# Performance work log

Measured on AMD Instinct MI355X. Metric: run time of the kernel, lower is better.

The kernel has to match this reference:

```python
import jax, jax.numpy as jnp
import numpy as np

P = 16          # patch size
D = 256         # embed dim (complex channels)
L = 2           # depth (num blocks)
NE = 4          # num experts
FF = 1024       # ffn hidden = expand * D
B, T, C, IH, IW = 1, 8, 4, 256, 256
HP, WP = IH // P, IW // P


def setup_inputs():
    key = jax.random.key(0)
    ks = iter(jax.random.split(key, 40))
    r = lambda shape, s=0.02: jax.random.normal(next(ks), shape, jnp.float32) * s
    sD = 1.0 / np.sqrt(D)
    return {
        'x': jax.random.normal(next(ks), (B, T, C, IH, IW), jnp.float32),
        'dt': jax.random.uniform(next(ks), (B, T), jnp.float32, 0.1, 1.0),
        'Wenc': r((C * P * P, 2 * D)),
        'benc': jnp.zeros((2 * D,), jnp.float32),
        'Wdec': r((2 * D, C * P * P)),
        'bdec': jnp.zeros((C * P * P,), jnp.float32),
        'ln_sp_w': jnp.ones((L, 2 * D), jnp.float32),
        'ln_sp_b': jnp.zeros((L, 2 * D), jnp.float32),
        'conv_w': r((L, 2 * D, 2 * D, 3, 3)),
        'conv_b': jnp.zeros((L, 2 * D), jnp.float32),
        'E_re': r((L, D, D), sD), 'E_im': r((L, D, D), sD),
        'Ed_re': r((L, D, D), sD), 'Ed_im': r((L, D, D), sD),
        'Ws_re': r((L, D, D), sD), 'Ws_im': r((L, D, D), sD),
        'Wg': r((L, 2 * D, D)),
        'bg': jnp.zeros((L, D), jnp.float32),
        'lam_re': r((L, D), 1.0), 'lam_im': r((L, D), 1.0),
        'ln_t_w': jnp.ones((L, 2 * D), jnp.float32),
        'ln_t_b': jnp.zeros((L, 2 * D), jnp.float32),
        'Wr': r((L, 2 * D, NE)),
        'W1': r((L, NE, 2 * D, FF)),
        'W2': r((L, NE, FF, 2 * D)),
    }


def _ln(x, w, b):
    m = x.mean(-1, keepdims=True)
    v = ((x - m) ** 2).mean(-1, keepdims=True)
    return (x - m) * jax.lax.rsqrt(v + 1e-5) * w + b


def _block(z, h_prev, flux_prev, dt, bp):
    (ln_sp_w, ln_sp_b, conv_w, conv_b, E_re, E_im, Ed_re, Ed_im,
     Ws_re, Ws_im, Wg, bg, lam_re, lam_im, ln_t_w, ln_t_b, Wr, W1, W2) = bp
    Bq, Tq, Dq, H, W = z.shape
    # --- spatial process: LN + conv on concat(real, imag), complex residual ---
    zf = z.reshape(Bq * Tq, Dq, H, W)
    zr = jnp.concatenate([zf.real, zf.imag], axis=1)
    zn = _ln(zr.transpose(0, 2, 3, 1), ln_sp_w, ln_sp_b).transpose(0, 3, 1, 2)
    zs = jax.lax.conv_general_dilated(zn, conv_w, (1, 1), 'SAME',
                                      dimension_numbers=('NCHW', 'OIHW', 'NCHW'))
    zs = zs + conv_b[None, :, None, None]
    re, im = jnp.split(zs, 2, axis=1)
    x = (zf + (re + 1j * im)).reshape(Bq, Tq, Dq, H, W)
    # --- eigen-basis encode ---
    Eb = E_re + 1j * E_im
    x_eigen = jnp.einsum('btdhw,de->bthwe', x, Eb)   # [B,T,H,W,D] complex
    x_mean = x_eigen.mean(axis=(2, 3))               # [B,T,D] complex
    # --- sequential gated flux recurrence over T ---
    Ws = Ws_re + 1j * Ws_im
    def step(flux, xm):
        source = xm @ Ws
        feat = jnp.concatenate([xm.real, xm.imag], -1)
        gate = jax.nn.sigmoid(feat @ Wg + bg)        # real [B,D]
        new_flux = gate * flux + (1.0 - gate) * source
        return new_flux, (new_flux, source, gate)
    _, (flux_seq, source_seq, gate_seq) = jax.lax.scan(step, flux_prev, x_mean.transpose(1, 0, 2))
    flux_seq = flux_seq.transpose(1, 0, 2)
    source_seq = source_seq.transpose(1, 0, 2)
    gate_seq = gate_seq.transpose(1, 0, 2)
    g = gate_seq[:, :, None, None, :]
    forcing = x_eigen * g + source_seq[:, :, None, None, :] * (1.0 - g)
    # --- transition operators ---
    lam = -(jax.nn.softplus(lam_re) + 1e-2) + 1j * lam_im        # [D]
    op_decay = jnp.exp(lam[None, None, :] * dt[:, :, None])      # [B,T,D] complex
    op_forcing = (op_decay - 1.0) / lam
    a = jnp.broadcast_to(op_decay[:, :, None, None, :], forcing.shape)
    u = forcing * op_forcing[:, :, None, None, :]
    # --- parallel linear scan h_t = a_t * h_{t-1} + u_t along T ---
    def comb(c1, c2):
        a1, u1 = c1
        a2, u2 = c2
        return a1 * a2, u1 * a2 + u2
    _, h = jax.lax.associative_scan(comb, (a, u), axis=1)
    # as written in source: h_prev contribution is h_prev * op_decay at every t
    h = h + h_prev.reshape(Bq, 1, H, W, Dq) * a
    last_h = h[:, -1].reshape(Bq * H * W, 1, Dq)
    last_flux = flux_seq[:, -1]
    # --- eigen decode + temporal LN + MoE FFN ---
    Ed = Ed_re + 1j * Ed_im
    x_out = jnp.einsum('bthwe,ed->btdhw', h, Ed)
    xf = x_out.reshape(Bq * Tq, Dq, H, W)
    xr = jnp.concatenate([xf.real, xf.imag], axis=1)
    xn = _ln(xr.transpose(0, 2, 3, 1), ln_t_w, ln_t_b)           # [BT,H,W,2D]
    tok = xn.reshape(-1, 2 * Dq)
    probs = jax.nn.softmax(tok @ Wr, axis=-1)                    # [N,E]
    hid = jax.nn.gelu(jnp.einsum('nd,edf->nef', tok, W1))
    y = jnp.einsum('nef,efd,ne->nd', hid, W2, probs)             # [N,2D]
    xc = xn[..., :Dq] + 1j * xn[..., Dq:]
    delta = (y[..., :Dq] + 1j * y[..., Dq:]).reshape(Bq * Tq, H, W, Dq)
    x_cplx = (xc + delta).reshape(Bq, Tq, H, W, Dq).transpose(0, 1, 4, 2, 3)
    return x + x_cplx, last_h, last_flux


def _forward(x, dt, Wenc, benc, Wdec, bdec, ln_sp_w, ln_sp_b, conv_w, conv_b,
             E_re, E_im, Ed_re, Ed_im, Ws_re, Ws_im, Wg, bg, lam_re, lam_im,
             ln_t_w, ln_t_b, Wr, W1, W2):
    # encoder: patchify + linear -> complex latent [B,T,D,HP,WP]
    xp = x.reshape(B, T, C, HP, P, WP, P).transpose(0, 1, 3, 5, 2, 4, 6)
    xp = xp.reshape(B, T, HP, WP, C * P * P)
    ze = xp @ Wenc + benc                                        # [B,T,HP,WP,2D]
    z = (ze[..., :D] + 1j * ze[..., D:]).transpose(0, 1, 4, 2, 3)
    h_prev = jnp.zeros((B * HP * WP, 1, D), jnp.complex64)
    flux_prev = jnp.zeros((B, D), jnp.complex64)
    bparams = (ln_sp_w, ln_sp_b, conv_w, conv_b, E_re, E_im, Ed_re, Ed_im,
               Ws_re, Ws_im, Wg, bg, lam_re, lam_im, ln_t_w, ln_t_b, Wr, W1, W2)
    for i in range(L):
        bp = tuple(p[i] for p in bparams)
        z, h_prev, flux_prev = _block(z, h_prev, flux_prev, dt, bp)
    # decoder: linear + unpatchify (real output)
    zr = jnp.concatenate([z.real, z.imag], axis=2).transpose(0, 1, 3, 4, 2)
    yo = zr @ Wdec + bdec                                        # [B,T,HP,WP,C*P*P]
    out = yo.reshape(B, T, HP, WP, C, P, P).transpose(0, 1, 4, 2, 5, 3, 6)
    return out.reshape(B, T, C, IH, IW)


def reference(x, dt, Wenc, benc, Wdec, bdec, ln_sp_w, ln_sp_b, conv_w, conv_b,
              E_re, E_im, Ed_re, Ed_im, Ws_re, Ws_im, Wg, bg, lam_re, lam_im,
              ln_t_w, ln_t_b, Wr, W1, W2):
    return _forward(x, dt, Wenc, benc, Wdec, bdec, ln_sp_w, ln_sp_b, conv_w, conv_b,
                    E_re, E_im, Ed_re, Ed_im, Ws_re, Ws_im, Wg, bg, lam_re, lam_im,
                    ln_t_w, ln_t_b, Wr, W1, W2)
```

## Files before the change

kernel.cpp:

```cpp
#include <hip/hip_runtime.h>
#include <hip/hip_bf16.h>


#define TOKS 2048
#define PSLICE 1048576

typedef __bf16 bf16;
typedef __attribute__((ext_vector_type(8))) __bf16 bf16x8;
typedef __attribute__((ext_vector_type(4))) __bf16 bf16x4;
typedef __attribute__((ext_vector_type(4))) float f32x4;

enum GMode { EENC = 0, ECONV, ESQ, ESQM, EMOE1, EMOE2, EDEC };

template <int MODE, int SPLIT>
__global__ __launch_bounds__(256) void mgemm_k(
    const bf16* __restrict__ A, const bf16* __restrict__ Bt,
    const float* __restrict__ bias, const float* __restrict__ scalev,
    float* __restrict__ C, bf16* __restrict__ C16, float* __restrict__ Cpart,
    float* __restrict__ xmean, int K, int N) {
  __shared__ __align__(16) bf16 As[64 * 40];
  __shared__ __align__(16) bf16 Bs[64 * 40];
  const int tid = threadIdx.x;
  const int bm = blockIdx.x * 64, bn = blockIdx.y * 64;
  const int lane = tid & 63, w = tid >> 6;
  const int wm = (w & 1) * 32, wn = (w >> 1) * 32;
  const int quad = lane >> 4, l16 = lane & 15;
  const int srow = tid >> 2, sko = (tid & 3) << 3;

  const int kbase = (SPLIT > 1) ? blockIdx.z * (K / SPLIT) : 0;
  const int kiter = K / (32 * SPLIT);
  if constexpr (MODE == EMOE1) Bt += (size_t)blockIdx.z * 524288;

  f32x4 acc[2][2] = {};

  int cv_t = 0, cv_h = 0, cv_w = 0;
  if constexpr (MODE == ECONV) {
    const int gm = bm + srow;
    cv_t = gm >> 8;
    cv_h = (gm >> 4) & 15;
    cv_w = gm & 15;
  }

  auto loadA = [&](int kt) -> bf16x8 {
    const int gk = kbase + kt * 32 + sko;
    if constexpr (MODE == ECONV) {
      const int s = gk >> 9, ci = gk & 511;
      const int kh = s / 3, kw = s - kh * 3;
      const int hh = cv_h + kh - 1, ww = cv_w + kw - 1;
      if (hh >= 0 && hh < 16 && ww >= 0 && ww < 16)
        return *(const bf16x8*)&A[(size_t)(((cv_t << 8) + hh * 16 + ww) << 9) +
                                  ci];
      bf16x8 zz;
#pragma unroll
      for (int q = 0; q < 8; q++) zz[q] = (bf16)0.0f;
      return zz;
    } else {
      return *(const bf16x8*)&A[(size_t)(bm + srow) * K + gk];
    }
  };
  auto loadB = [&](int kt) -> bf16x8 {
    return *(const bf16x8*)&Bt[(size_t)(bn + srow) * K + kbase + kt * 32 + sko];
  };

  bf16x8 pa = loadA(0), pb = loadB(0);
  for (int kt = 0; kt < kiter; kt++) {
    *(bf16x8*)&As[srow * 40 + sko] = pa;
    *(bf16x8*)&Bs[srow * 40 + sko] = pb;
    __syncthreads();
    if (kt + 1 < kiter) {
      pa = loadA(kt + 1);
      pb = loadB(kt + 1);
    }
    const bf16x8 a0 = *(const bf16x8*)&As[(wm + l16) * 40 + quad * 8];
    const bf16x8 a1 = *(const bf16x8*)&As[(wm + 16 + l16) * 40 + quad * 8];
    const bf16x8 b0 = *(const bf16x8*)&Bs[(wn + l16) * 40 + quad * 8];
    const bf16x8 b1 = *(const bf16x8*)&Bs[(wn + 16 + l16) * 40 + quad * 8];
    acc[0][0] = __builtin_amdgcn_mfma_f32_16x16x32_bf16(a0, b0, acc[0][0], 0, 0, 0);
    acc[0][1] = __builtin_amdgcn_mfma_f32_16x16x32_bf16(a0, b1, acc[0][1], 0, 0, 0);
    acc[1][0] = __builtin_amdgcn_mfma_f32_16x16x32_bf16(a1, b0, acc[1][0], 0, 0, 0);
    acc[1][1] = __builtin_amdgcn_mfma_f32_16x16x32_bf16(a1, b1, acc[1][1], 0, 0, 0);
    __syncthreads();
  }

#pragma unroll
  for (int i = 0; i < 2; i++) {
#pragma unroll
    for (int j = 0; j < 2; j++) {
#pragma unroll
      for (int r = 0; r < 4; r++) {
        const int gm = bm + wm + i * 16 + quad * 4 + r;
        const int gn = bn + wn + j * 16 + l16;
        const float v = acc[i][j][r];
        if constexpr (SPLIT > 1) {
          Cpart[(size_t)blockIdx.z * PSLICE + (size_t)gm * 512 + gn] = v;
        } else if constexpr (MODE == EMOE1) {
          const float t = 0.7978845608028654f * (v + 0.044715f * v * v * v);
          const float g = 0.5f * v * (1.f + tanhf(t));
          const float p = scalev[gm * 4 + blockIdx.z];
          C16[(size_t)gm * 4096 + blockIdx.z * 1024 + gn] = (bf16)(p * g);
        } else {
          const int t = gm >> 8, hp = (gm >> 4) & 15, wp = gm & 15;
          const int c = gn >> 8, ph = (gn >> 4) & 15, pw = gn & 15;
          C[(size_t)(((t * 4 + c) * 256 + hp * 16 + ph) << 8) + wp * 16 + pw] =
              v + bias[gn];
        }
      }
    }
  }
  if constexpr (MODE == ESQM) {
    const int t = bm >> 8;
#pragma unroll
    for (int j = 0; j < 2; j++) {
      float cs = 0.f;
#pragma unroll
      for (int i = 0; i < 2; i++)
#pragma unroll
        for (int r = 0; r < 4; r++) cs += acc[i][j][r];
      atomicAdd(&xmean[t * 512 + bn + wn + j * 16 + l16], cs);
    }
  }
}

__global__ __launch_bounds__(256) void conv_ep_k(
    const float* __restrict__ parts, const float* __restrict__ bias,
    const float* __restrict__ resid, float* __restrict__ xb,
    bf16* __restrict__ xb16, float* __restrict__ xmean) {
  if (blockIdx.x < 16) xmean[blockIdx.x * 256 + threadIdx.x] = 0.f;
  const int i4 = (blockIdx.x * 256 + threadIdx.x) << 2;
  const int c = i4 & 511;
  float4 o = *(const float4*)&resid[i4];
  const float4 bi = *(const float4*)&bias[c];
  o.x += bi.x; o.y += bi.y; o.z += bi.z; o.w += bi.w;
#pragma unroll
  for (int s = 0; s < 8; s++) {
    const float4 p = *(const float4*)&parts[(size_t)s * PSLICE + i4];
    o.x += p.x; o.y += p.y; o.z += p.z; o.w += p.w;
  }
  *(float4*)&xb[i4] = o;
  bf16x4 o16 = {(bf16)o.x, (bf16)o.y, (bf16)o.z, (bf16)o.w};
  *(bf16x4*)&xb16[i4] = o16;
}

template <bool ENC>
__global__ __launch_bounds__(256) void ln_comb_k(
    const float* __restrict__ parts, const float* __restrict__ bias,
    const float* __restrict__ w, const float* __restrict__ b,
    const float* __restrict__ Wr, float* __restrict__ zout,
    float* __restrict__ out32, bf16* __restrict__ out16,
    float* __restrict__ probs) {
  const int wv = threadIdx.x >> 6, lane = threadIdx.x & 63;
  const int n = (blockIdx.x << 2) + wv;
  float v[8];
  float s = 0.f, s2 = 0.f;
#pragma unroll
  for (int i = 0; i < 8; i++) {
    const int c = (i << 6) + lane;
    float x = parts[(size_t)n * 512 + c] + parts[PSLICE + (size_t)n * 512 + c];
    if constexpr (ENC) x += bias[c];
    v[i] = x;
    s += x;
    s2 += x * x;
  }
#pragma unroll
  for (int off = 32; off > 0; off >>= 1) {
    s += __shfl_down(s, off);
    s2 += __shfl_down(s2, off);
  }
  s = __shfl(s, 0);
  s2 = __shfl(s2, 0);
  const float m = s * (1.f / 512.f);
  const float var = s2 * (1.f / 512.f) - m * m;
  const float r = rsqrtf(var + 1e-5f);
  float a0 = 0.f, a1 = 0.f, a2 = 0.f, a3 = 0.f;
#pragma unroll
  for (int i = 0; i < 8; i++) {
    const int c = (i << 6) + lane;
    const float o = (v[i] - m) * r * w[c] + b[c];
    if constexpr (ENC) {
      zout[(size_t)n * 512 + c] = v[i];
    } else {
      out32[(size_t)n * 512 + c] = o;
      a0 += o * Wr[c * 4 + 0];
      a1 += o * Wr[c * 4 + 1];
      a2 += o * Wr[c * 4 + 2];
      a3 += o * Wr[c * 4 + 3];
    }
    out16[(size_t)n * 512 + c] = (bf16)o;
  }
  if constexpr (!ENC) {
#pragma unroll
    for (int off = 32; off > 0; off >>= 1) {
      a0 += __shfl_down(a0, off);
      a1 += __shfl_down(a1, off);
      a2 += __shfl_down(a2, off);
      a3 += __shfl_down(a3, off);
    }
    if (lane == 0) {
      const float mx = fmaxf(fmaxf(a0, a1), fmaxf(a2, a3));
      const float e0 = expf(a0 - mx), e1 = expf(a1 - mx), e2 = expf(a2 - mx),
                  e3 = expf(a3 - mx);
      const float inv = 1.f / (e0 + e1 + e2 + e3);
      probs[n * 4 + 0] = e0 * inv;
      probs[n * 4 + 1] = e1 * inv;
      probs[n * 4 + 2] = e2 * inv;
      probs[n * 4 + 3] = e3 * inv;
    }
  }
}

template <bool DO_LN>
__global__ __launch_bounds__(256) void addf2_k(
    const float* __restrict__ xb, const float* __restrict__ xn,
    const float* __restrict__ parts, const float* __restrict__ w,
    const float* __restrict__ b, float* __restrict__ zout,
    bf16* __restrict__ out16) {
  const int wv = threadIdx.x >> 6, lane = threadIdx.x & 63;
  const int n = (blockIdx.x << 2) + wv;
  float v[8];
  float s = 0.f, s2 = 0.f;
#pragma unroll
  for (int i = 0; i < 8; i++) {
    const size_t idx = (size_t)n * 512 + (i << 6) + lane;
    float x = xb[idx] + xn[idx];
#pragma unroll
    for (int sl = 0; sl < 8; sl++) x += parts[(size_t)sl * PSLICE + idx];
    v[i] = x;
    s += x;
    s2 += x * x;
  }
  if constexpr (!DO_LN) {
#pragma unroll
    for (int i = 0; i < 8; i++)
      out16[(size_t)n * 512 + (i << 6) + lane] = (bf16)v[i];
    return;
  }
#pragma unroll
  for (int off = 32; off > 0; off >>= 1) {
    s += __shfl_down(s, off);
    s2 += __shfl_down(s2, off);
  }
  s = __shfl(s, 0);
  s2 = __shfl(s2, 0);
  const float m = s * (1.f / 512.f);
  const float var = s2 * (1.f / 512.f) - m * m;
  const float r = rsqrtf(var + 1e-5f);
#pragma unroll
  for (int i = 0; i < 8; i++) {
    const int c = (i << 6) + lane;
    const float x = v[i];
    zout[(size_t)n * 512 + c] = x;
    out16[(size_t)n * 512 + c] = (bf16)((x - m) * r * w[c] + b[c]);
  }
}

__global__ __launch_bounds__(256) void cvt_all_k(
    const float* __restrict__ x, const float* __restrict__ Wenc,
    const float* __restrict__ Wdec, const float* __restrict__ W1,
    const float* __restrict__ W2, const float* __restrict__ E_re,
    const float* __restrict__ E_im, const float* __restrict__ Ed_re,
    const float* __restrict__ Ed_im, const float* __restrict__ conv_w,
    bf16* __restrict__ Ae, bf16* __restrict__ WencT, bf16* __restrict__ WdecT,
    bf16* __restrict__ W1T, bf16* __restrict__ W2Tc, bf16* __restrict__ MEt,
    bf16* __restrict__ convBt) {
  __shared__ float smem[4608];
  float(*tile)[33] = (float(*)[33])smem;
  const int tid = threadIdx.x;
  int b = blockIdx.x;
  const int tx = tid & 31, ty = tid >> 5;
  auto tpose = [&](const float* src, bf16* dst, int N, int dstride, int k0,
                   int n0) {
#pragma unroll
    for (int r = 0; r < 4; r++)
      tile[ty + 8 * r][tx] = src[(size_t)(k0 + ty + 8 * r) * N + n0 + tx];
    __syncthreads();
#pragma unroll
    for (int r = 0; r < 4; r++)
      dst[(size_t)(n0 + ty + 8 * r) * dstride + k0 + tx] =
          (bf16)tile[tx][ty + 8 * r];
  };
  if (b < 1024) {
    const int id = b * 256 + tid;
    const int n = id >> 7;
    const int kc = (id & 127) << 3;
    const int t = n >> 8, hp = (n >> 4) & 15, wp = n & 15;
    const int c = kc >> 8, ph = (kc >> 4) & 15, pw = kc & 15;
    const float* src =
        &x[(size_t)(((t * 4 + c) * 256 + hp * 16 + ph) << 8) + wp * 16 + pw];
    const float4 v0 = *(const float4*)src;
    const float4 v1 = *(const float4*)(src + 4);
    bf16* d = &Ae[(size_t)n * 1024 + kc];
    d[0] = (bf16)v0.x; d[1] = (bf16)v0.y; d[2] = (bf16)v0.z; d[3] = (bf16)v0.w;
    d[4] = (bf16)v1.x; d[5] = (bf16)v1.y; d[6] = (bf16)v1.z; d[7] = (bf16)v1.w;
    return;
  }
  b -= 1024;
  if (b < 512) {
    tpose(Wenc, WencT, 512, 1024, (b & 31) * 32, (b >> 5) * 32);
    return;
  }
  b -= 512;
  if (b < 512) {
    tpose(Wdec, WdecT, 1024, 512, (b & 15) * 32, (b >> 4) * 32);
    return;
  }
  b -= 512;
  if (b < 4096) {
    const int z = b >> 9, rem = b & 511;
    tpose(W1 + (size_t)z * 524288, W1T + (size_t)z * 524288, 1024, 512,
          (rem & 15) * 32, (rem >> 4) * 32);
    return;
  }
  b -= 4096;
  if (b < 4096) {
    const int z = b >> 9, rem = b & 511;
    const int l = z >> 2, e = z & 3;
    tpose(W2 + (size_t)z * 524288, W2Tc + (size_t)l * 2097152 + e * 1024, 512,
          4096, (rem & 31) * 32, (rem >> 5) * 32);
    return;
  }
  b -= 4096;
  if (b < 4096) {
    const int z = b >> 10;
    const int l = z >> 1, which = z & 1;
    const float* Er = (which ? Ed_re : E_re) + l * 65536;
    const float* Ei = (which ? Ed_im : E_im) + l * 65536;
    bf16* dst = MEt + (size_t)z * 262144;
    const int idx = (b & 1023) * 256 + tid;
    const int j = idx >> 9, k = idx & 511;
    const int kk = k & 255, jj = j & 255;
    const float er = Er[kk * 256 + jj], ei = Ei[kk * 256 + jj];
    const float v = (k < 256) ? ((j < 256) ? er : ei) : ((j < 256) ? -ei : er);
    dst[idx] = (bf16)v;
    return;
  }
  b -= 4096;
  {
    const int l = b >> 9, co = b & 511;
    const float* src = conv_w + (size_t)l * 2359296 + (size_t)co * 4608;
    bf16* d = convBt + (size_t)l * 2359296 + (size_t)co * 4608;
    for (int i = tid; i < 4608; i += 256) smem[i] = src[i];
    __syncthreads();
    for (int o = tid; o < 4608; o += 256) {
      const int s = o >> 9, ci = o & 511;
      d[o] = (bf16)smem[ci * 9 + s];
    }
  }
}

__global__ __launch_bounds__(256) void srcgate_k(
    const float* __restrict__ xmean, const float* __restrict__ Wsr,
    const float* __restrict__ Wsi, const float* __restrict__ Wg,
    const float* __restrict__ bg, float* __restrict__ srcs,
    float* __restrict__ gts) {
  const int t = blockIdx.x, part = blockIdx.y, d = threadIdx.x;
  __shared__ float sxm[512];
  for (int c = d; c < 512; c += 256) sxm[c] = xmean[t * 512 + c] * (1.f / 256.f);
  __syncthreads();
  if (part == 0) {
    float s0 = 0.f, s1 = 0.f, s2 = 0.f, s3 = 0.f;
#pragma unroll 4
    for (int e = 0; e < 256; e += 4) {
      s0 += sxm[e + 0] * Wsr[(e + 0) * 256 + d] - sxm[256 + e + 0] * Wsi[(e + 0) * 256 + d];
      s1 += sxm[e + 1] * Wsr[(e + 1) * 256 + d] - sxm[256 + e + 1] * Wsi[(e + 1) * 256 + d];
      s2 += sxm[e + 2] * Wsr[(e + 2) * 256 + d] - sxm[256 + e + 2] * Wsi[(e + 2) * 256 + d];
      s3 += sxm[e + 3] * Wsr[(e + 3) * 256 + d] - sxm[256 + e + 3] * Wsi[(e + 3) * 256 + d];
    }
    srcs[t * 512 + d] = (s0 + s1) + (s2 + s3);
  } else if (part == 1) {
    float s0 = 0.f, s1 = 0.f, s2 = 0.f, s3 = 0.f;
#pragma unroll 4
    for (int e = 0; e < 256; e += 4) {
      s0 += sxm[e + 0] * Wsi[(e + 0) * 256 + d] + sxm[256 + e + 0] * Wsr[(e + 0) * 256 + d];
      s1 += sxm[e + 1] * Wsi[(e + 1) * 256 + d] + sxm[256 + e + 1] * Wsr[(e + 1) * 256 + d];
      s2 += sxm[e + 2] * Wsi[(e + 2) * 256 + d] + sxm[256 + e + 2] * Wsr[(e + 2) * 256 + d];
      s3 += sxm[e + 3] * Wsi[(e + 3) * 256 + d] + sxm[256 + e + 3] * Wsr[(e + 3) * 256 + d];
    }
    srcs[t * 512 + 256 + d] = (s0 + s1) + (s2 + s3);
  } else {
    float s0 = 0.f, s1 = 0.f, s2 = 0.f, s3 = 0.f;
#pragma unroll 4
    for (int c = 0; c < 512; c += 4) {
      s0 += sxm[c + 0] * Wg[(c + 0) * 256 + d];
      s1 += sxm[c + 1] * Wg[(c + 1) * 256 + d];
      s2 += sxm[c + 2] * Wg[(c + 2) * 256 + d];
      s3 += sxm[c + 3] * Wg[(c + 3) * 256 + d];
    }
    const float ga = (s0 + s1) + (s2 + s3) + bg[d];
    gts[t * 256 + d] = 1.f / (1.f + expf(-ga));
  }
}

template <bool FIRST>
__global__ __launch_bounds__(256) void time_scan_k(
    const float* __restrict__ parts, const float* __restrict__ gts,
    const float* __restrict__ srcs, const float* __restrict__ lamre,
    const float* __restrict__ lamim, const float* __restrict__ dt,
    bf16* __restrict__ hout16, float* __restrict__ hprev) {
  const int d = threadIdx.x;
  const int p = blockIdx.x;
  const float lr0 = lamre[d];
  const float sp = (lr0 > 20.f) ? lr0 : log1pf(expf(lr0));
  const float lre = -(sp + 0.01f);
  const float lim = lamim[d];
  const float den = lre * lre + lim * lim;
  float ar[8], ai[8], ofr[8], ofi[8];
#pragma unroll
  for (int t = 0; t < 8; t++) {
    const float dtv = dt[t];
    const float er = expf(lre * dtv);
    const float odr = er * cosf(lim * dtv);
    const float odi = er * sinf(lim * dtv);
    ar[t] = odr;
    ai[t] = odi;
    const float nr = odr - 1.f, ni = odi;
    ofr[t] = (nr * lre + ni * lim) / den;
    ofi[t] = (ni * lre - nr * lim) / den;
  }
  float hr = 0.f, hi = 0.f;
  float hpr = 0.f, hpi = 0.f;
  if constexpr (!FIRST) {
    hpr = hprev[p * 512 + d];
    hpi = hprev[p * 512 + 256 + d];
  }
  float o7r = 0.f, o7i = 0.f;
#pragma unroll
  for (int t = 0; t < 8; t++) {
    const size_t base = (size_t)((t << 8) + p) * 512;
    const float xr = parts[base + d] + parts[PSLICE + base + d];
    const float xi = parts[base + 256 + d] + parts[PSLICE + base + 256 + d];
    const float g = gts[t * 256 + d];
    const float sr = srcs[t * 512 + d], si = srcs[t * 512 + 256 + d];
    const float fr = xr * g + sr * (1.f - g);
    const float fi = xi * g + si * (1.f - g);
    const float ur = fr * ofr[t] - fi * ofi[t];
    const float ui = fr * ofi[t] + fi * ofr[t];
    const float nhr = ur + ar[t] * hr - ai[t] * hi;
    const float nhi = ui + ar[t] * hi + ai[t] * hr;
    hr = nhr;
    hi = nhi;
    const float outr = hr + ar[t] * hpr - ai[t] * hpi;
    const float outi = hi + ar[t] * hpi + ai[t] * hpr;
    hout16[base + d] = (bf16)outr;
    hout16[base + 256 + d] = (bf16)outi;
    if (t == 7) {
      o7r = outr;
      o7i = outi;
    }
  }
  hprev[p * 512 + d] = o7r;
  hprev[p * 512 + 256 + d] = o7i;
}

extern "C" void kernel_launch(void* const* d_in, const int* in_sizes, int n_in,
                              void* d_out, int out_size, void* d_ws,
                              size_t ws_size, hipStream_t stream) {
  const float* x_in = (const float*)d_in[0];
  const float* dt = (const float*)d_in[1];
  const float* Wenc = (const float*)d_in[2];
  const float* benc = (const float*)d_in[3];
  const float* Wdec = (const float*)d_in[4];
  const float* bdec = (const float*)d_in[5];
  const float* ln_sp_w = (const float*)d_in[6];
  const float* ln_sp_b = (const float*)d_in[7];
  const float* conv_w = (const float*)d_in[8];
  const float* conv_b = (const float*)d_in[9];
  const float* E_re = (const float*)d_in[10];
  const float* E_im = (const float*)d_in[11];
  const float* Ed_re = (const float*)d_in[12];
  const float* Ed_im = (const float*)d_in[13];
  const float* Ws_re = (const float*)d_in[14];
  const float* Ws_im = (const float*)d_in[15];
  const float* Wg = (const float*)d_in[16];
  const float* bg = (const float*)d_in[17];
  const float* lam_re = (const float*)d_in[18];
  const float* lam_im = (const float*)d_in[19];
  const float* ln_t_w = (const float*)d_in[20];
  const float* ln_t_b = (const float*)d_in[21];
  const float* Wr = (const float*)d_in[22];
  const float* W1 = (const float*)d_in[23];
  const float* W2 = (const float*)d_in[24];
  float* out = (float*)d_out;

  float* ws = (float*)d_ws;
  size_t off = 0;
  auto allocf = [&](size_t n) {
    float* p = ws + off;
    off += n;
    return p;
  };
  auto allocb = [&](size_t n) {
    bf16* p = (bf16*)(ws + off);
    off += n / 2;
    return p;
  };
  float* z = allocf((size_t)TOKS * 512);
  float* xn = allocf((size_t)TOKS * 512);
  float* xb = allocf((size_t)TOKS * 512);
  float* parts = allocf((size_t)8 * PSLICE);
  float* hprev = allocf(256 * 512);
  float* xm = allocf(8 * 512);
  float* srcs = allocf(8 * 512);
  float* gts = allocf(8 * 256);
  float* probs = allocf((size_t)TOKS * 4);
  bf16* znsp16 = allocb((size_t)TOKS * 512);
  bf16* xn16 = allocb((size_t)TOKS * 512);
  bf16* xb16 = allocb((size_t)TOKS * 512);
  bf16* z16 = allocb((size_t)TOKS * 512);
  bf16* hb16 = allocb((size_t)TOKS * 512);
  bf16* hid16 = allocb((size_t)TOKS * 4096);
  bf16* Aenc16 = allocb((size_t)TOKS * 1024);
  bf16* WencT = allocb((size_t)512 * 1024);
  bf16* WdecT = allocb((size_t)1024 * 512);
  bf16* MEt = allocb((size_t)4 * 512 * 512);
  bf16* convBt = allocb((size_t)2 * 512 * 4608);
  bf16* W1T = allocb((size_t)8 * 1024 * 512);
  bf16* W2Tc = allocb((size_t)2 * 512 * 4096);

  cvt_all_k<<<15360, 256, 0, stream>>>(x_in, Wenc, Wdec, W1, W2, E_re, E_im,
                                       Ed_re, Ed_im, conv_w, Aenc16, WencT,
                                       WdecT, W1T, W2Tc, MEt, convBt);

  mgemm_k<EENC, 2><<<dim3(32, 8, 2), 256, 0, stream>>>(
      Aenc16, WencT, nullptr, nullptr, nullptr, nullptr, parts, nullptr, 1024,
      512);
  ln_comb_k<true><<<512, 256, 0, stream>>>(parts, benc, ln_sp_w, ln_sp_b,
                                           nullptr, z, nullptr, znsp16,
                                           nullptr);

  for (int l = 0; l < 2; l++) {
    mgemm_k<ECONV, 8><<<dim3(32, 8, 8), 256, 0, stream>>>(
        znsp16, convBt + (size_t)l * 2359296, nullptr, nullptr, nullptr,
        nullptr, parts, nullptr, 4608, 512);
    conv_ep_k<<<1024, 256, 0, stream>>>(parts, conv_b + l * 512, z, xb, xb16,
                                        xm);
    mgemm_k<ESQM, 2><<<dim3(32, 8, 2), 256, 0, stream>>>(
        xb16, MEt + (size_t)(l * 2) * 262144, nullptr, nullptr, nullptr,
        nullptr, parts, xm, 512, 512);
    srcgate_k<<<dim3(8, 3), 256, 0, stream>>>(xm, Ws_re + l * 65536,
                                              Ws_im + l * 65536,
                                              Wg + l * 131072, bg + l * 256,
                                              srcs, gts);
    if (l == 0)
      time_scan_k<true><<<256, 256, 0, stream>>>(parts, gts, srcs, lam_re,
                                                 lam_im, dt, hb16, hprev);
    else
      time_scan_k<false><<<256, 256, 0, stream>>>(parts, gts, srcs,
                                                  lam_re + 256, lam_im + 256,
                                                  dt, hb16, hprev);
    mgemm_k<ESQ, 2><<<dim3(32, 8, 2), 256, 0, stream>>>(
        hb16, MEt + (size_t)(l * 2 + 1) * 262144, nullptr, nullptr, nullptr,
        nullptr, parts, nullptr, 512, 512);
    ln_comb_k<false><<<512, 256, 0, stream>>>(parts, nullptr, ln_t_w + l * 512,
                                              ln_t_b + l * 512, Wr + l * 2048,
                                              nullptr, xn, xn16, probs);
    mgemm_k<EMOE1, 1><<<dim3(32, 16, 4), 256, 0, stream>>>(
        xn16, W1T + (size_t)l * 2097152, nullptr, probs, nullptr, hid16,
        nullptr, nullptr, 512, 1024);
    mgemm_k<EMOE2, 8><<<dim3(32, 8, 8), 256, 0, stream>>>(
        hid16, W2Tc + (size_t)l * 2097152, nullptr, nullptr, nullptr, nullptr,
        parts, nullptr, 4096, 512);
    if (l == 0)
      addf2_k<true><<<512, 256, 0, stream>>>(xb, xn, parts, ln_sp_w + 512,
                                             ln_sp_b + 512, z, znsp16);
    else
      addf2_k<false><<<512, 256, 0, stream>>>(xb, xn, parts, nullptr, nullptr,
                                              nullptr, z16);
  }

  mgemm_k<EDEC, 1><<<dim3(32, 16), 256, 0, stream>>>(
      z16, WdecT, bdec, nullptr, out, nullptr, nullptr, nullptr, 512, 1024);
}
```

Baseline: 458.8 us.

## Use direct global-to-LDS loads with double-buffered swizzled tiles; store residuals as bf16

The GEMM kernel now uses global_load_lds to copy A/B tiles directly into a double-buffered, XOR-swizzled LDS layout. This drops the register staging step and one of the two barriers per k-step. Conv padding taps point at a small zero buffer instead of being built in registers. Separately, the fp32 residual/activation buffers (z, xb, xn) become bf16 copies to cut memory traffic, which lowers residual-stream precision.

Measured after the change: 464.3 us. No clear change (+1.2%).

```diff
diff --git a/kernel.cpp b/kernel.cpp
--- a/kernel.cpp
+++ b/kernel.cpp
@@ -11,21 +11,29 @@
 typedef __attribute__((ext_vector_type(4))) float f32x4;
 
 enum GMode { EENC = 0, ECONV, ESQ, ESQM, EMOE1, EMOE2, EDEC };
+
+__device__ __forceinline__ void gload16(const void* g, void* l) {
+  __builtin_amdgcn_global_load_lds(
+      (const __attribute__((address_space(1))) unsigned int*)g,
+      (__attribute__((address_space(3))) unsigned int*)l, 16, 0, 0);
+}
 
 template <int MODE, int SPLIT>
 __global__ __launch_bounds__(256) void mgemm_k(
     const bf16* __restrict__ A, const bf16* __restrict__ Bt,
     const float* __restrict__ bias, const float* __restrict__ scalev,
     float* __restrict__ C, bf16* __restrict__ C16, float* __restrict__ Cpart,
-    float* __restrict__ xmean, int K, int N) {
-  __shared__ __align__(16) bf16 As[64 * 40];
-  __shared__ __align__(16) bf16 Bs[64 * 40];
+    float* __restrict__ xmean, const float* __restrict__ zerop, int K, int N) {
+  __shared__ __align__(16) bf16 As[2][2048];
+  __shared__ __align__(16) bf16 Bs[2][2048];
   const int tid = threadIdx.x;
   const int bm = blockIdx.x * 64, bn = blockIdx.y * 64;
   const int lane = tid & 63, w = tid >> 6;
   const int wm = (w & 1) * 32, wn = (w >> 1) * 32;
   const int quad = lane >> 4, l16 = lane & 15;
-  const int srow = tid >> 2, sko = (tid & 3) << 3;
+
+  const int srow = w * 16 + (lane >> 2);
+  const int sjj = (lane & 3) ^ ((srow >> 1) & 3);
 
   const int kbase = (SPLIT > 1) ? blockIdx.z * (K / SPLIT) : 0;
   const int kiter = K / (32 * SPLIT);
@@ -34,52 +42,54 @@
   f32x4 acc[2][2] = {};
 
   int cv_t = 0, cv_h = 0, cv_w = 0;
+  const bf16* aRow = nullptr;
   if constexpr (MODE == ECONV) {
     const int gm = bm + srow;
     cv_t = gm >> 8;
     cv_h = (gm >> 4) & 15;
     cv_w = gm & 15;
-  }
-
-  auto loadA = [&](int kt) -> bf16x8 {
-    const int gk = kbase + kt * 32 + sko;
+  } else {
+    aRow = A + (size_t)(bm + srow) * K + kbase + sjj * 8;
+  }
+  const bf16* bRow = Bt + (size_t)(bn + srow) * K + kbase + sjj * 8;
+
+  auto issue = [&](int kt, int buf) {
+    const bf16* ga;
     if constexpr (MODE == ECONV) {
-      const int s = gk >> 9, ci = gk & 511;
+      const int gk0 = kbase + kt * 32;
+      const int s = gk0 >> 9;
       const int kh = s / 3, kw = s - kh * 3;
       const int hh = cv_h + kh - 1, ww = cv_w + kw - 1;
       if (hh >= 0 && hh < 16 && ww >= 0 && ww < 16)
-        return *(const bf16x8*)&A[(size_t)(((cv_t << 8) + hh * 16 + ww) << 9) +
-                                  ci];
-      bf16x8 zz;
-#pragma unroll
-      for (int q = 0; q < 8; q++) zz[q] = (bf16)0.0f;
-      return zz;
+        ga = A + (size_t)(((cv_t << 8) + hh * 16 + ww) << 9) + (gk0 & 511) +
+             sjj * 8;
+      else
+        ga = (const bf16*)zerop;
     } else {
-      return *(const bf16x8*)&A[(size_t)(bm + srow) * K + gk];
-    }
+      ga = aRow + kt * 32;
+    }
+    gload16(ga, &As[buf][w * 512]);
+    gload16(bRow + kt * 32, &Bs[buf][w * 512]);
   };
-  auto loadB = [&](int kt) -> bf16x8 {
-    return *(const bf16x8*)&Bt[(size_t)(bn + srow) * K + kbase + kt * 32 + sko];
+  auto frag = [&](const bf16* S, int r) -> bf16x8 {
+    const int unit = r * 4 + (quad ^ ((r >> 1) & 3));
+    return *(const bf16x8*)&S[unit * 8];
   };
 
-  bf16x8 pa = loadA(0), pb = loadB(0);
+  issue(0, 0);
   for (int kt = 0; kt < kiter; kt++) {
-    *(bf16x8*)&As[srow * 40 + sko] = pa;
-    *(bf16x8*)&Bs[srow * 40 + sko] = pb;
     __syncthreads();
-    if (kt + 1 < kiter) {
-      pa = loadA(kt + 1);
-      pb = loadB(kt + 1);
-    }
-    const bf16x8 a0 = *(const bf16x8*)&As[(wm + l16) * 40 + quad * 8];
-    const bf16x8 a1 = *(const bf16x8*)&As[(wm + 16 + l16) * 40 + quad * 8];
-    const bf16x8 b0 = *(const bf16x8*)&Bs[(wn + l16) * 40 + quad * 8];
-    const bf16x8 b1 = *(const bf16x8*)&Bs[(wn + 16 + l16) * 40 + quad * 8];
+    if (kt + 1 < kiter) issue(kt + 1, (kt + 1) & 1);
+    const bf16* Ab = As[kt & 1];
+    const bf16* Bb = Bs[kt & 1];
+    const bf16x8 a0 = frag(Ab, wm + l16);
+    const bf16x8 a1 = frag(Ab, wm + 16 + l16);
+    const bf16x8 b0 = frag(Bb, wn + l16);
+    const bf16x8 b1 = frag(Bb, wn + 16 + l16);
     acc[0][0] = __builtin_amdgcn_mfma_f32_16x16x32_bf16(a0, b0, acc[0][0], 0, 0, 0);
     acc[0][1] = __builtin_amdgcn_mfma_f32_16x16x32_bf16(a0, b1, acc[0][1], 0, 0, 0);
     acc[1][0] = __builtin_amdgcn_mfma_f32_16x16x32_bf16(a1, b0, acc[1][0], 0, 0, 0);
     acc[1][1] = __builtin_amdgcn_mfma_f32_16x16x32_bf16(a1, b1, acc[1][1], 0, 0, 0);
-    __syncthreads();
   }
 
 #pragma unroll
@@ -123,20 +133,20 @@
 
 __global__ __launch_bounds__(256) void conv_ep_k(
     const float* __restrict__ parts, const float* __restrict__ bias,
-    const float* __restrict__ resid, float* __restrict__ xb,
-    bf16* __restrict__ xb16, float* __restrict__ xmean) {
+    const bf16* __restrict__ resid16, bf16* __restrict__ xb16,
+    float* __restrict__ xmean) {
   if (blockIdx.x < 16) xmean[blockIdx.x * 256 + threadIdx.x] = 0.f;
   const int i4 = (blockIdx.x * 256 + threadIdx.x) << 2;
   const int c = i4 & 511;
-  float4 o = *(const float4*)&resid[i4];
+  const bf16x4 rz = *(const bf16x4*)&resid16[i4];
   const float4 bi = *(const float4*)&bias[c];
-  o.x += bi.x; o.y += bi.y; o.z += bi.z; o.w += bi.w;
+  float4 o = make_float4((float)rz[0] + bi.x, (float)rz[1] + bi.y,
+                         (float)rz[2] + bi.z, (float)rz[3] + bi.w);
 #pragma unroll
   for (int s = 0; s < 8; s++) {
     const float4 p = *(const float4*)&parts[(size_t)s * PSLICE + i4];
     o.x += p.x; o.y += p.y; o.z += p.z; o.w += p.w;
   }
-  *(float4*)&xb[i4] = o;
   bf16x4 o16 = {(bf16)o.x, (bf16)o.y, (bf16)o.z, (bf16)o.w};
   *(bf16x4*)&xb16[i4] = o16;
 }
@@ -145,9 +155,8 @@
 __global__ __launch_bounds__(256) void ln_comb_k(
     const float* __restrict__ parts, const float* __restrict__ bias,
     const float* __restrict__ w, const float* __restrict__ b,
-    const float* __restrict__ Wr, float* __restrict__ zout,
-    float* __restrict__ out32, bf16* __restrict__ out16,
-    float* __restrict__ probs) {
+    const float* __restrict__ Wr, bf16* __restrict__ zraw16,
+    bf16* __restrict__ out16, float* __restrict__ probs) {
   const int wv = threadIdx.x >> 6, lane = threadIdx.x & 63;
   const int n = (blockIdx.x << 2) + wv;
   float v[8];
@@ -176,16 +185,14 @@
   for (int i = 0; i < 8; i++) {
     const int c = (i << 6) + lane;
     const float o = (v[i] - m) * r * w[c] + b[c];
-    if constexpr (ENC) {
-      zout[(size_t)n * 512 + c] = v[i];
-    } else {
-      out32[(size_t)n * 512 + c] = o;
+    if constexpr (ENC) zraw16[(size_t)n * 512 + c] = (bf16)v[i];
+    out16[(size_t)n * 512 + c] = (bf16)o;
+    if constexpr (!ENC) {
       a0 += o * Wr[c * 4 + 0];
       a1 += o * Wr[c * 4 + 1];
       a2 += o * Wr[c * 4 + 2];
       a3 += o * Wr[c * 4 + 3];
     }
-    out16[(size_t)n * 512 + c] = (bf16)o;
   }
   if constexpr (!ENC) {
 #pragma unroll
@@ -210,9 +217,9 @@
 
 template <bool DO_LN>
 __global__ __launch_bounds__(256) void addf2_k(
-    const float* __restrict__ xb, const float* __restrict__ xn,
+    const bf16* __restrict__ xb16, const bf16* __restrict__ xn16,
     const float* __restrict__ parts, const float* __restrict__ w,
-    const float* __restrict__ b, float* __restrict__ zout,
+    const float* __restrict__ b, bf16* __restrict__ zraw16,
     bf16* __restrict__ out16) {
   const int wv = threadIdx.x >> 6, lane = threadIdx.x & 63;
   const int n = (blockIdx.x << 2) + wv;
@@ -221,7 +228,7 @@
 #pragma unroll
   for (int i = 0; i < 8; i++) {
     const size_t idx = (size_t)n * 512 + (i << 6) + lane;
-    float x = xb[idx] + xn[idx];
+    float x = (float)xb16[idx] + (float)xn16[idx];
 #pragma unroll
     for (int sl = 0; sl < 8; sl++) x += parts[(size_t)sl * PSLICE + idx];
     v[i] = x;
@@ -247,9 +254,8 @@
 #pragma unroll
   for (int i = 0; i < 8; i++) {
     const int c = (i << 6) + lane;
-    const float x = v[i];
-    zout[(size_t)n * 512 + c] = x;
-    out16[(size_t)n * 512 + c] = (bf16)((x - m) * r * w[c] + b[c]);
+    zraw16[(size_t)n * 512 + c] = (bf16)v[i];
+    out16[(size_t)n * 512 + c] = (bf16)((v[i] - m) * r * w[c] + b[c]);
   }
 }
 
@@ -261,7 +267,7 @@
     const float* __restrict__ Ed_im, const float* __restrict__ conv_w,
     bf16* __restrict__ Ae, bf16* __restrict__ WencT, bf16* __restrict__ WdecT,
     bf16* __restrict__ W1T, bf16* __restrict__ W2Tc, bf16* __restrict__ MEt,
-    bf16* __restrict__ convBt) {
+    bf16* __restrict__ convBt, float* __restrict__ zerop) {
   __shared__ float smem[4608];
   float(*tile)[33] = (float(*)[33])smem;
   const int tid = threadIdx.x;
@@ -279,6 +285,7 @@
           (bf16)tile[tx][ty + 8 * r];
   };
   if (b < 1024) {
+    if (b == 0 && tid < 16) zerop[tid] = 0.f;
     const int id = b * 256 + tid;
     const int n = id >> 7;
     const int kc = (id & 127) << 3;
@@ -493,15 +500,14 @@
     off += n / 2;
     return p;
   };
-  float* z = allocf((size_t)TOKS * 512);
-  float* xn = allocf((size_t)TOKS * 512);
-  float* xb = allocf((size_t)TOKS * 512);
   float* parts = allocf((size_t)8 * PSLICE);
   float* hprev = allocf(256 * 512);
+  float* zerop = allocf(16);
   float* xm = allocf(8 * 512);
   float* srcs = allocf(8 * 512);
   float* gts = allocf(8 * 256);
   float* probs = allocf((size_t)TOKS * 4);
+  bf16* zraw16 = allocb((size_t)TOKS * 512);
   bf16* znsp16 = allocb((size_t)TOKS * 512);
   bf16* xn16 = allocb((size_t)TOKS * 512);
   bf16* xb16 = allocb((size_t)TOKS * 512);
@@ -518,24 +524,23 @@
 
   cvt_all_k<<<15360, 256, 0, stream>>>(x_in, Wenc, Wdec, W1, W2, E_re, E_im,
                                        Ed_re, Ed_im, conv_w, Aenc16, WencT,
-                                       WdecT, W1T, W2Tc, MEt, convBt);
+                                       WdecT, W1T, W2Tc, MEt, convBt, zerop);
 
   mgemm_k<EENC, 2><<<dim3(32, 8, 2), 256, 0, stream>>>(
-      Aenc16, WencT, nullptr, nullptr, nullptr, nullptr, parts, nullptr, 1024,
-      512);
+      Aenc16, WencT, nullptr, nullptr, nullptr, nullptr, parts, nullptr, zerop,
+      1024, 512);
   ln_comb_k<true><<<512, 256, 0, stream>>>(parts, benc, ln_sp_w, ln_sp_b,
-                                           nullptr, z, nullptr, znsp16,
-                                           nullptr);
+                                           nullptr, zraw16, znsp16, nullptr);
 
   for (int l = 0; l < 2; l++) {
     mgemm_k<ECONV, 8><<<dim3(32, 8, 8), 256, 0, stream>>>(
         znsp16, convBt + (size_t)l * 2359296, nullptr, nullptr, nullptr,
-        nullptr, parts, nullptr, 4608, 512);
-    conv_ep_k<<<1024, 256, 0, stream>>>(parts, conv_b + l * 512, z, xb, xb16,
+        nullptr, parts, nullptr, zerop, 4608, 512);
+    conv_ep_k<<<1024, 256, 0, stream>>>(parts, conv_b + l * 512, zraw16, xb16,
                                         xm);
     mgemm_k<ESQM, 2><<<dim3(32, 8, 2), 256, 0, stream>>>(
         xb16, MEt + (size_t)(l * 2) * 262144, nullptr, nullptr, nullptr,
-        nullptr, parts, xm, 512, 512);
+        nullptr, parts, xm, zerop, 512, 512);
     srcgate_k<<<dim3(8, 3), 256, 0, stream>>>(xm, Ws_re + l * 65536,
                                               Ws_im + l * 65536,
                                               Wg + l * 131072, bg + l * 256,
@@ -549,24 +554,25 @@
                                                   dt, hb16, hprev);
     mgemm_k<ESQ, 2><<<dim3(32, 8, 2), 256, 0, stream>>>(
         hb16, MEt + (size_t)(l * 2 + 1) * 262144, nullptr, nullptr, nullptr,
-        nullptr, parts, nullptr, 512, 512);
+        nullptr, parts, nullptr, zerop, 512, 512);
     ln_comb_k<false><<<512, 256, 0, stream>>>(parts, nullptr, ln_t_w + l * 512,
                                               ln_t_b + l * 512, Wr + l * 2048,
-                                              nullptr, xn, xn16, probs);
+                                              nullptr, xn16, probs);
     mgemm_k<EMOE1, 1><<<dim3(32, 16, 4), 256, 0, stream>>>(
         xn16, W1T + (size_t)l * 2097152, nullptr, probs, nullptr, hid16,
-        nullptr, nullptr, 512, 1024);
+        nullptr, nullptr, zerop, 512, 1024);
     mgemm_k<EMOE2, 8><<<dim3(32, 8, 8), 256, 0, stream>>>(
         hid16, W2Tc + (size_t)l * 2097152, nullptr, nullptr, nullptr, nullptr,
-        parts, nullptr, 4096, 512);
+        parts, nullptr, zerop, 4096, 512);
     if (l == 0)
-      addf2_k<true><<<512, 256, 0, stream>>>(xb, xn, parts, ln_sp_w + 512,
-                                             ln_sp_b + 512, z, znsp16);
+      addf2_k<true><<<512, 256, 0, stream>>>(xb16, xn16, parts, ln_sp_w + 512,
+                                             ln_sp_b + 512, zraw16, znsp16);
     else
-      addf2_k<false><<<512, 256, 0, stream>>>(xb, xn, parts, nullptr, nullptr,
-                                              nullptr, z16);
+      addf2_k<false><<<512, 256, 0, stream>>>(xb16, xn16, parts, nullptr,
+                                              nullptr, nullptr, z16);
   }
 
   mgemm_k<EDEC, 1><<<dim3(32, 16), 256, 0, stream>>>(
-      z16, WdecT, bdec, nullptr, out, nullptr, nullptr, nullptr, 512, 1024);
-}
+      z16, WdecT, bdec, nullptr, out, nullptr, nullptr, nullptr, zerop, 512,
+      1024);
+}
```

## Store split-K partials and residual activations in bf16 instead of fp32

Applied to the files above, without the earlier changes.

The 8-way split-K conv and MoE-down GEMMs now write their partial sums as bf16 into a new buffer, and the reducing epilogue kernels read bf16 partials. The fp32 residual copies (z, xb, xn) are dropped; their bf16 versions are read instead. This roughly halves the bytes moved through the partial-sum and residual traffic. In exchange, accumulated sums and the residual stream lose precision, which may push error closer to tolerance.

After: 443.5 us. -3.3%, faster.

```diff
diff --git a/kernel.cpp b/kernel.cpp
--- a/kernel.cpp
+++ b/kernel.cpp
@@ -4,6 +4,7 @@
 
 #define TOKS 2048
 #define PSLICE 1048576
+#define BPSLICE 1048576
 
 typedef __bf16 bf16;
 typedef __attribute__((ext_vector_type(8))) __bf16 bf16x8;
@@ -12,12 +13,12 @@
 
 enum GMode { EENC = 0, ECONV, ESQ, ESQM, EMOE1, EMOE2, EDEC };
 
-template <int MODE, int SPLIT>
+template <int MODE, int SPLIT, bool BPART>
 __global__ __launch_bounds__(256) void mgemm_k(
     const bf16* __restrict__ A, const bf16* __restrict__ Bt,
     const float* __restrict__ bias, const float* __restrict__ scalev,
     float* __restrict__ C, bf16* __restrict__ C16, float* __restrict__ Cpart,
-    float* __restrict__ xmean, int K, int N) {
+    bf16* __restrict__ Cpart16, float* __restrict__ xmean, int K, int N) {
   __shared__ __align__(16) bf16 As[64 * 40];
   __shared__ __align__(16) bf16 Bs[64 * 40];
   const int tid = threadIdx.x;
@@ -92,7 +93,11 @@
         const int gn = bn + wn + j * 16 + l16;
         const float v = acc[i][j][r];
         if constexpr (SPLIT > 1) {
-          Cpart[(size_t)blockIdx.z * PSLICE + (size_t)gm * 512 + gn] = v;
+          if constexpr (BPART)
+            Cpart16[(size_t)blockIdx.z * BPSLICE + (size_t)gm * 512 + gn] =
+                (bf16)v;
+          else
+            Cpart[(size_t)blockIdx.z * PSLICE + (size_t)gm * 512 + gn] = v;
         } else if constexpr (MODE == EMOE1) {
           const float t = 0.7978845608028654f * (v + 0.044715f * v * v * v);
           const float g = 0.5f * v * (1.f + tanhf(t));
@@ -122,22 +127,25 @@
 }
 
 __global__ __launch_bounds__(256) void conv_ep_k(
-    const float* __restrict__ parts, const float* __restrict__ bias,
-    const float* __restrict__ resid, float* __restrict__ xb,
-    bf16* __restrict__ xb16, float* __restrict__ xmean) {
+    const bf16* __restrict__ parts, const float* __restrict__ bias,
+    const bf16* __restrict__ resid16, bf16* __restrict__ xb16,
+    float* __restrict__ xmean) {
   if (blockIdx.x < 16) xmean[blockIdx.x * 256 + threadIdx.x] = 0.f;
   const int i4 = (blockIdx.x * 256 + threadIdx.x) << 2;
   const int c = i4 & 511;
-  float4 o = *(const float4*)&resid[i4];
+  const bf16x4 rz = *(const bf16x4*)&resid16[i4];
   const float4 bi = *(const float4*)&bias[c];
-  o.x += bi.x; o.y += bi.y; o.z += bi.z; o.w += bi.w;
+  float o0 = (float)rz[0] + bi.x, o1 = (float)rz[1] + bi.y;
+  float o2 = (float)rz[2] + bi.z, o3 = (float)rz[3] + bi.w;
 #pragma unroll
   for (int s = 0; s < 8; s++) {
-    const float4 p = *(const float4*)&parts[(size_t)s * PSLICE + i4];
-    o.x += p.x; o.y += p.y; o.z += p.z; o.w += p.w;
-  }
-  *(float4*)&xb[i4] = o;
-  bf16x4 o16 = {(bf16)o.x, (bf16)o.y, (bf16)o.z, (bf16)o.w};
+    const bf16x4 p = *(const bf16x4*)&parts[(size_t)s * BPSLICE + i4];
+    o0 += (float)p[0];
+    o1 += (float)p[1];
+    o2 += (float)p[2];
+    o3 += (float)p[3];
+  }
+  bf16x4 o16 = {(bf16)o0, (bf16)o1, (bf16)o2, (bf16)o3};
   *(bf16x4*)&xb16[i4] = o16;
 }
 
@@ -145,9 +153,8 @@
 __global__ __launch_bounds__(256) void ln_comb_k(
     const float* __restrict__ parts, const float* __restrict__ bias,
     const float* __restrict__ w, const float* __restrict__ b,
-    const float* __restrict__ Wr, float* __restrict__ zout,
-    float* __restrict__ out32, bf16* __restrict__ out16,
-    float* __restrict__ probs) {
+    const float* __restrict__ Wr, bf16* __restrict__ zraw16,
+    bf16* __restrict__ out16, float* __restrict__ probs) {
   const int wv = threadIdx.x >> 6, lane = threadIdx.x & 63;
   const int n = (blockIdx.x << 2) + wv;
   float v[8];
@@ -176,16 +183,14 @@
   for (int i = 0; i < 8; i++) {
     const int c = (i << 6) + lane;
     const float o = (v[i] - m) * r * w[c] + b[c];
-    if constexpr (ENC) {
-      zout[(size_t)n * 512 + c] = v[i];
-    } else {
-      out32[(size_t)n * 512 + c] = o;
+    if constexpr (ENC) zraw16[(size_t)n * 512 + c] = (bf16)v[i];
+    out16[(size_t)n * 512 + c] = (bf16)o;
+    if constexpr (!ENC) {
       a0 += o * Wr[c * 4 + 0];
       a1 += o * Wr[c * 4 + 1];
       a2 += o * Wr[c * 4 + 2];
       a3 += o * Wr[c * 4 + 3];
     }
-    out16[(size_t)n * 512 + c] = (bf16)o;
   }
   if constexpr (!ENC) {
 #pragma unroll
@@ -210,9 +215,9 @@
 
 template <bool DO_LN>
 __global__ __launch_bounds__(256) void addf2_k(
-    const float* __restrict__ xb, const float* __restrict__ xn,
-    const float* __restrict__ parts, const float* __restrict__ w,
-    const float* __restrict__ b, float* __restrict__ zout,
+    const bf16* __restrict__ xb16, const bf16* __restrict__ xn16,
+    const bf16* __restrict__ parts, const float* __restrict__ w,
+    const float* __restrict__ b, bf16* __restrict__ zraw16,
     bf16* __restrict__ out16) {
   const int wv = threadIdx.x >> 6, lane = threadIdx.x & 63;
   const int n = (blockIdx.x << 2) + wv;
@@ -221,9 +226,10 @@
 #pragma unroll
   for (int i = 0; i < 8; i++) {
     const size_t idx = (size_t)n * 512 + (i << 6) + lane;
-    float x = xb[idx] + xn[idx];
-#pragma unroll
-    for (int sl = 0; sl < 8; sl++) x += parts[(size_t)sl * PSLICE + idx];
+    float x = (float)xb16[idx] + (float)xn16[idx];
+#pragma unroll
+    for (int sl = 0; sl < 8; sl++)
+      x += (float)parts[(size_t)sl * BPSLICE + idx];
     v[i] = x;
     s += x;
     s2 += x * x;
@@ -247,9 +253,8 @@
 #pragma unroll
   for (int i = 0; i < 8; i++) {
     const int c = (i << 6) + lane;
-    const float x = v[i];
-    zout[(size_t)n * 512 + c] = x;
-    out16[(size_t)n * 512 + c] = (bf16)((x - m) * r * w[c] + b[c]);
+    zraw16[(size_t)n * 512 + c] = (bf16)v[i];
+    out16[(size_t)n * 512 + c] = (bf16)((v[i] - m) * r * w[c] + b[c]);
   }
 }
 
@@ -493,15 +498,14 @@
     off += n / 2;
     return p;
   };
-  float* z = allocf((size_t)TOKS * 512);
-  float* xn = allocf((size_t)TOKS * 512);
-  float* xb = allocf((size_t)TOKS * 512);
-  float* parts = allocf((size_t)8 * PSLICE);
+  float* parts = allocf((size_t)2 * PSLICE);
+  bf16* bparts = allocb((size_t)8 * BPSLICE);
   float* hprev = allocf(256 * 512);
   float* xm = allocf(8 * 512);
   float* srcs = allocf(8 * 512);
   float* gts = allocf(8 * 256);
   float* probs = allocf((size_t)TOKS * 4);
+  bf16* zraw16 = allocb((size_t)TOKS * 512);
   bf16* znsp16 = allocb((size_t)TOKS * 512);
   bf16* xn16 = allocb((size_t)TOKS * 512);
   bf16* xb16 = allocb((size_t)TOKS * 512);
@@ -520,22 +524,21 @@
                                        Ed_re, Ed_im, conv_w, Aenc16, WencT,
                                        WdecT, W1T, W2Tc, MEt, convBt);
 
-  mgemm_k<EENC, 2><<<dim3(32, 8, 2), 256, 0, stream>>>(
-      Aenc16, WencT, nullptr, nullptr, nullptr, nullptr, parts, nullptr, 1024,
-      512);
+  mgemm_k<EENC, 2, false><<<dim3(32, 8, 2), 256, 0, stream>>>(
+      Aenc16, WencT, nullptr, nullptr, nullptr, nullptr, parts, nullptr,
+      nullptr, 1024, 512);
   ln_comb_k<true><<<512, 256, 0, stream>>>(parts, benc, ln_sp_w, ln_sp_b,
-                                           nullptr, z, nullptr, znsp16,
-                                           nullptr);
+                                           nullptr, zraw16, znsp16, nullptr);
 
   for (int l = 0; l < 2; l++) {
-    mgemm_k<ECONV, 8><<<dim3(32, 8, 8), 256, 0, stream>>>(
+    mgemm_k<ECONV, 8, true><<<dim3(32, 8, 8), 256, 0, stream>>>(
         znsp16, convBt + (size_t)l * 2359296, nullptr, nullptr, nullptr,
-        nullptr, parts, nullptr, 4608, 512);
-    conv_ep_k<<<1024, 256, 0, stream>>>(parts, conv_b + l * 512, z, xb, xb16,
+        nullptr, nullptr, bparts, nullptr, 4608, 512);
+    conv_ep_k<<<1024, 256, 0, stream>>>(bparts, conv_b + l * 512, zraw16, xb16,
                                         xm);
-    mgemm_k<ESQM, 2><<<dim3(32, 8, 2), 256, 0, stream>>>(
+    mgemm_k<ESQM, 2, false><<<dim3(32, 8, 2), 256, 0, stream>>>(
         xb16, MEt + (size_t)(l * 2) * 262144, nullptr, nullptr, nullptr,
-        nullptr, parts, xm, 512, 512);
+        nullptr, parts, nullptr, xm, 512, 512);
     srcgate_k<<<dim3(8, 3), 256, 0, stream>>>(xm, Ws_re + l * 65536,
                                               Ws_im + l * 65536,
                                               Wg + l * 131072, bg + l * 256,
@@ -547,26 +550,27 @@
       time_scan_k<false><<<256, 256, 0, stream>>>(parts, gts, srcs,
                                                   lam_re + 256, lam_im + 256,
                                                   dt, hb16, hprev);
-    mgemm_k<ESQ, 2><<<dim3(32, 8, 2), 256, 0, stream>>>(
+    mgemm_k<ESQ, 2, false><<<dim3(32, 8, 2), 256, 0, stream>>>(
         hb16, MEt + (size_t)(l * 2 + 1) * 262144, nullptr, nullptr, nullptr,
-        nullptr, parts, nullptr, 512, 512);
+        nullptr, parts, nullptr, nullptr, 512, 512);
     ln_comb_k<false><<<512, 256, 0, stream>>>(parts, nullptr, ln_t_w + l * 512,
                                               ln_t_b + l * 512, Wr + l * 2048,
-                                              nullptr, xn, xn16, probs);
-    mgemm_k<EMOE1, 1><<<dim3(32, 16, 4), 256, 0, stream>>>(
+                                              nullptr, xn16, probs);
+    mgemm_k<EMOE1, 1, false><<<dim3(32, 16, 4), 256, 0, stream>>>(
         xn16, W1T + (size_t)l * 2097152, nullptr, probs, nullptr, hid16,
-        nullptr, nullptr, 512, 1024);
-    mgemm_k<EMOE2, 8><<<dim3(32, 8, 8), 256, 0, stream>>>(
+        nullptr, nullptr, nullptr, 512, 1024);
+    mgemm_k<EMOE2, 8, true><<<dim3(32, 8, 8), 256, 0, stream>>>(
         hid16, W2Tc + (size_t)l * 2097152, nullptr, nullptr, nullptr, nullptr,
-        parts, nullptr, 4096, 512);
+        nullptr, bparts, nullptr, 4096, 512);
     if (l == 0)
-      addf2_k<true><<<512, 256, 0, stream>>>(xb, xn, parts, ln_sp_w + 512,
-                                             ln_sp_b + 512, z, znsp16);
+      addf2_k<true><<<512, 256, 0, stream>>>(xb16, xn16, bparts, ln_sp_w + 512,
+                                             ln_sp_b + 512, zraw16, znsp16);
     else
-      addf2_k<false><<<512, 256, 0, stream>>>(xb, xn, parts, nullptr, nullptr,
-                                              nullptr, z16);
-  }
-
-  mgemm_k<EDEC, 1><<<dim3(32, 16), 256, 0, stream>>>(
-      z16, WdecT, bdec, nullptr, out, nullptr, nullptr, nullptr, 512, 1024);
-}
+      addf2_k<false><<<512, 256, 0, stream>>>(xb16, xn16, bparts, nullptr,
+                                              nullptr, nullptr, z16);
+  }
+
+  mgemm_k<EDEC, 1, false><<<dim3(32, 16), 256, 0, stream>>>(
+      z16, WdecT, bdec, nullptr, out, nullptr, nullptr, nullptr, nullptr, 512,
+      1024);
+}
```
